# Optimization experiments

Measured on AMD Instinct MI355X. Metric: run time of the kernel, lower is better.

## Reference

```python
import jax, jax.numpy as jnp
import numpy as np

DIM = 768
HID = 1536
EPS = 1e-12
SCALE = float(np.sqrt(DIM))


def _layernorm(x, gamma, beta):
    mu = jnp.mean(x, axis=-1, keepdims=True)
    var = jnp.mean(jnp.square(x - mu), axis=-1, keepdims=True)
    return (x - mu) * jax.lax.rsqrt(var + EPS) * gamma + beta


def setup_inputs() -> dict:
    key = jax.random.key(0)
    ks = jax.random.split(key, 16)
    s = 1.0 / np.sqrt(DIM)
    sh = 1.0 / np.sqrt(HID)
    x = jax.random.normal(ks[0], (8, 2048, DIM), dtype=jnp.float32)
    return {
        "x": x,
        "Wq": jax.random.uniform(ks[1], (DIM, DIM), jnp.float32, -s, s),
        "bq": jax.random.uniform(ks[2], (DIM,), jnp.float32, -s, s),
        "Wk": jax.random.uniform(ks[3], (DIM, DIM), jnp.float32, -s, s),
        "bk": jax.random.uniform(ks[4], (DIM,), jnp.float32, -s, s),
        "Wv": jax.random.uniform(ks[5], (DIM, DIM), jnp.float32, -s, s),
        "bv": jax.random.uniform(ks[6], (DIM,), jnp.float32, -s, s),
        "Wp": jax.random.uniform(ks[7], (DIM, DIM), jnp.float32, -s, s),
        "bp": jax.random.uniform(ks[8], (DIM,), jnp.float32, -s, s),
        "g1": jnp.ones((DIM,), jnp.float32),
        "be1": jnp.zeros((DIM,), jnp.float32),
        "W1": jax.random.uniform(ks[9], (HID, DIM), jnp.float32, -s, s),
        "b1": jax.random.uniform(ks[10], (HID,), jnp.float32, -s, s),
        "W2": jax.random.uniform(ks[11], (DIM, HID), jnp.float32, -sh, sh),
        "b2": jax.random.uniform(ks[12], (DIM,), jnp.float32, -sh, sh),
        "g2": jnp.ones((DIM,), jnp.float32),
        "be2": jnp.zeros((DIM,), jnp.float32),
    }


def reference(x, Wq, bq, Wk, bk, Wv, bv, Wp, bp, g1, be1, W1, b1, W2, b2, g2, be2):
    # NOTE: original code does NOT split into heads; single full-dim bmm attention.
    Q = jnp.einsum("bsd,ed->bse", x, Wq) + bq  # [B,S,D]
    K = jnp.einsum("bsd,ed->bse", x, Wk) + bk
    V = jnp.einsum("bsd,ed->bse", x, Wv) + bv
    alpha = jnp.einsum("bqd,bkd->bqk", Q, K) / SCALE  # [B,S,S]
    alpha = jax.nn.softmax(alpha, axis=-1)
    attn = jnp.einsum("bqk,bkd->bqd", alpha, V)
    attn = jnp.einsum("bsd,ed->bse", attn, Wp) + bp  # linear_proj
    h = _layernorm(x + attn, g1, be1)
    mlp = jax.nn.gelu(jnp.einsum("bsd,hd->bsh", h, W1) + b1, approximate=False)
    mlp = jnp.einsum("bsh,dh->bsd", mlp, W2) + b2
    return _layernorm(h + mlp, g2, be2)
```

## Files before the change

### kernel.cpp

```cpp
#include <hip/hip_runtime.h>
#include <math.h>

#define D_MODEL 768
#define D_HID   1536
#define N_BATCH 8
#define SEQLEN  2048
#define NROWS   (N_BATCH*SEQLEN)

typedef unsigned short u16;
typedef unsigned char  u8;
typedef __attribute__((ext_vector_type(8))) short bfrag;
typedef __attribute__((ext_vector_type(4))) float facc;

__device__ __forceinline__ u16 f2bf(float f) {
  unsigned u = __float_as_uint(f);
  u += 0x7fffu + ((u >> 16) & 1u);
  return (u16)(u >> 16);
}
__device__ __forceinline__ float bf2f(u16 u) {
  return __uint_as_float((unsigned)u << 16);
}
__device__ __forceinline__ u8 f2fp8(float f) {
  return (u8)(__builtin_amdgcn_cvt_pk_fp8_f32(f, f, 0, 0) & 0xff);
}

__device__ __forceinline__ void async16(const void* g, void* l) {
  __builtin_amdgcn_global_load_lds((const __attribute__((address_space(1))) void*)g,
                                   (__attribute__((address_space(3))) void*)l,
                                   16, 0, 0);
}

__global__ __launch_bounds__(256) void cvt_all(
    const float* __restrict__ x,  const float* __restrict__ Wq,
    const float* __restrict__ Wk, const float* __restrict__ Wv,
    const float* __restrict__ Wp, const float* __restrict__ W1,
    const float* __restrict__ W2, const float* __restrict__ bq,
    const float* __restrict__ bk, const float* __restrict__ bv,
    u16* __restrict__ XB, u16* __restrict__ WQKV, u16* __restrict__ WPB,
    u16* __restrict__ W1B, u16* __restrict__ W2B, float* __restrict__ BQKV,
    float* __restrict__ LSUM) {
  long i = (long)blockIdx.x * 256 + threadIdx.x;
  const float* src; u16* dst; long off;
  if      (i < 3145728) { src = x;  dst = XB;             off = i; }
  else if (i < 3293184) { src = Wq; dst = WQKV;           off = i - 3145728; }
  else if (i < 3440640) { src = Wk; dst = WQKV + 589824;  off = i - 3293184; }
  else if (i < 3588096) { src = Wv; dst = WQKV + 1179648; off = i - 3440640; }
  else if (i < 3735552) { src = Wp; dst = WPB;            off = i - 3588096; }
  else if (i < 4030464) { src = W1; dst = W1B;            off = i - 3735552; }
  else if (i < 4325376) { src = W2; dst = W2B;            off = i - 4030464; }
  else if (i < 4325952) {
    long j = i - 4325376;
    const float* s = (j < 192) ? bq : (j < 384) ? bk : bv;
    long o = (j < 192) ? j : (j < 384) ? j - 192 : j - 384;
    ((float4*)BQKV)[j] = ((const float4*)s)[o];
    return;
  } else if (i < 4330048) {
    float4 zz = {0.f, 0.f, 0.f, 0.f};
    ((float4*)LSUM)[i - 4325952] = zz;
    return;
  } else return;
  float4 v = ((const float4*)src)[off];
  ushort4 o4;
  o4.x = f2bf(v.x); o4.y = f2bf(v.y); o4.z = f2bf(v.z); o4.w = f2bf(v.w);
  *reinterpret_cast<ushort4*>(dst + off * 4) = o4;
}

enum { EPI_EXP = 1, EPI_DIV = 2, EPI_GELU = 4, EPI_QKV = 5, EPI_RES = 6 };

template<int EPI>
__global__ __launch_bounds__(512, 4)
void gemm_bt(const u16* __restrict__ Aall, const u16* __restrict__ Ball,
             void* __restrict__ Cout,
             int M, int N, int K,
             long sA, long sB, long sC,
             const float* __restrict__ bias,
             const u16* __restrict__ resid,
             float* __restrict__ lsum,
             float scale)
{
  __shared__ __align__(16) char smem[65536];
  u16* As = (u16*)smem;
  u16* Bs = (u16*)(smem + 16384);

  const int z = blockIdx.z;
  const u16* A = Aall + (long)z * sA;
  const u16* B = Ball + (long)z * sB;
  const int bm = blockIdx.x, bn = blockIdx.y;
  const int tid = (int)threadIdx.x;
  const int lane = tid & 63, wv = tid >> 6;
  const int wr = wv >> 2, wc = wv & 3;

  facc acc[4][4] = {};

  const int srow = tid >> 3;
  const int scol = (((tid & 7) ^ (srow & 7)) << 3);
  const u16* Abase = A + (long)(bm * 128) * K;
  const u16* Bbase = B + (long)(bn * 256) * K;

  const int fr = lane & 15;
  const int g0 = lane >> 4;

  for (int k0 = 0; k0 < K; k0 += 64) {
    __syncthreads();
#pragma unroll
    for (int p = 0; p < 2; ++p)
      async16(Abase + (long)(p * 64 + srow) * K + k0 + scol, As + (p * 512 + wv * 64) * 8);
#pragma unroll
    for (int p = 0; p < 4; ++p)
      async16(Bbase + (long)(p * 64 + srow) * K + k0 + scol, Bs + (p * 512 + wv * 64) * 8);
    __syncthreads();
#pragma unroll
    for (int h = 0; h < 2; ++h) {
      bfrag af[4], bfv[4];
      const int gh = g0 + h * 4;
#pragma unroll
      for (int i = 0; i < 4; ++i) {
        const int r = wr * 64 + i * 16 + fr;
        af[i] = *(const bfrag*)(As + r * 64 + ((gh ^ (r & 7)) << 3));
      }
#pragma unroll
      for (int j = 0; j < 4; ++j) {
        const int r = wc * 64 + j * 16 + fr;
        bfv[j] = *(const bfrag*)(Bs + r * 64 + ((gh ^ (r & 7)) << 3));
      }
#pragma unroll
      for (int i = 0; i < 4; ++i)
#pragma unroll
        for (int j = 0; j < 4; ++j)
          acc[i][j] = __builtin_amdgcn_mfma_f32_16x16x32_bf16(af[i], bfv[j], acc[i][j], 0, 0, 0);
    }
  }

  __syncthreads();
  const int rb = bm * 128 + wr * 64;
  const int cb = bn * 256 + wc * 64;
  const int quad = lane >> 4;

  if constexpr (EPI == EPI_QKV) {
    const int c64 = bn * 4 + wc;
    const int which = c64 / 12;
    float bj[4];
#pragma unroll
    for (int j = 0; j < 4; ++j) bj[j] = bias[cb + j * 16 + fr];
    if (which == 2) {
      u8* VT_ = (u8*)resid;
      const int zb = rb >> 11;
      const int seqb = (rb & 2047) + quad * 4;
      const int dimb = (c64 - 24) * 64;
#pragma unroll
      for (int i = 0; i < 4; ++i) {
#pragma unroll
        for (int j = 0; j < 4; ++j) {
          const int dim = dimb + j * 16 + fr;
          unsigned v01 = __builtin_amdgcn_cvt_pk_fp8_f32(acc[i][j][0] + bj[j],
                                                         acc[i][j][1] + bj[j], 0, 0);
          unsigned v23 = __builtin_amdgcn_cvt_pk_fp8_f32(acc[i][j][2] + bj[j],
                                                         acc[i][j][3] + bj[j], 0, 0);
          unsigned w = (v01 & 0xffffu) | (v23 << 16);
          *reinterpret_cast<unsigned*>(VT_ + (long)zb * D_MODEL * SEQLEN +
                                       (long)dim * SEQLEN + seqb + i * 16) = w;
        }
      }
      return;
    }
    u8* ep8 = (u8*)(smem + wv * 8192);
    u8* Cg = (u8*)Cout + (long)which * NROWS * D_MODEL;
    const int cbo = (c64 - which * 12) * 64;
#pragma unroll
    for (int i = 0; i < 4; ++i)
#pragma unroll
      for (int r = 0; r < 4; ++r) {
        const int lrow = i * 16 + quad * 4 + r;
#pragma unroll
        for (int j = 0; j < 4; ++j)
          ep8[lrow * 64 + j * 16 + fr] = f2fp8(acc[i][j][r] + bj[j]);
      }
#pragma unroll
    for (int it = 0; it < 4; ++it) {
      const int lr = it * 16 + (lane >> 2);
      const int ch = (lane & 3) << 4;
      int4 d = *(const int4*)(ep8 + lr * 64 + ch);
      *reinterpret_cast<int4*>(Cg + (long)(rb + lr) * D_MODEL + cbo + ch) = d;
    }
  } else {
    u16* ep16 = (u16*)(smem + wv * 8192);
    u16* Cg = (u16*)Cout + (long)z * sC;
    float bj[4];
#pragma unroll
    for (int j = 0; j < 4; ++j) bj[j] = bias[cb + j * 16 + fr];
#pragma unroll
    for (int i = 0; i < 4; ++i) {
#pragma unroll
      for (int r = 0; r < 4; ++r) {
        const int lrow = i * 16 + quad * 4 + r;
#pragma unroll
        for (int j = 0; j < 4; ++j) {
          float t = acc[i][j][r] + bj[j];
          float y = 0.7978845608f * (t + 0.044715f * t * t * t);
          float e = __expf(-2.f * fabsf(y));
          float th = (1.f - e) / (1.f + e);
          th = (y < 0.f) ? -th : th;
          ep16[lrow * 64 + j * 16 + fr] = f2bf(0.5f * t * (1.f + th));
        }
      }
    }
#pragma unroll
    for (int it = 0; it < 8; ++it) {
      const int lr = it * 8 + (lane >> 3);
      const int ch = (lane & 7) << 3;
      int4 d = *(const int4*)(ep16 + lr * 64 + ch);
      *reinterpret_cast<int4*>(Cg + (long)(rb + lr) * N + cb + ch) = d;
    }
  }
}

template<int EPI>
__global__ __launch_bounds__(512, 4)
void gemm_f8(const u8* __restrict__ Aall, const u8* __restrict__ Ball,
             void* __restrict__ Cout,
             int M, int N, int K,
             long sA, long sB, long sC,
             float* __restrict__ lsum, float scale)
{
  __shared__ __align__(16) char smem[49152];
  u8* As = (u8*)smem;
  u8* Bs = (u8*)(smem + 16384);

  const int z = blockIdx.z;
  const u8* A = Aall + (long)z * sA;
  const u8* B = Ball + (long)z * sB;
  const int bm = blockIdx.x, bn = blockIdx.y;
  const int tid = (int)threadIdx.x;
  const int lane = tid & 63, wv = tid >> 6;
  const int wr = wv >> 2, wc = wv & 3;

  facc acc[4][4] = {};

  const int srow = tid >> 3;
  const int scol = (((tid & 7) ^ (srow & 7)) << 4);
  const u8* Abase = A + (long)(bm * 128) * K;
  const u8* Bbase = B + (long)(bn * 256) * K;

  const int fr = lane & 15;
  const int g0 = lane >> 4;

  for (int k0 = 0; k0 < K; k0 += 128) {
    __syncthreads();
#pragma unroll
    for (int p = 0; p < 2; ++p)
      async16(Abase + (long)(p * 64 + srow) * K + k0 + scol, As + (p * 512 + wv * 64) * 16);
#pragma unroll
    for (int p = 0; p < 4; ++p)
      async16(Bbase + (long)(p * 64 + srow) * K + k0 + scol, Bs + (p * 512 + wv * 64) * 16);
    __syncthreads();
#pragma unroll
    for (int s = 0; s < 4; ++s) {
      long af[4], bfv[4];
      const int c = s * 2 + (g0 >> 1);
      const int w8 = (g0 & 1) << 3;
#pragma unroll
      for (int i = 0; i < 4; ++i) {
        const int r = wr * 64 + i * 16 + fr;
        af[i] = *(const long*)(As + r * 128 + ((c ^ (r & 7)) << 4) + w8);
      }
#pragma unroll
      for (int j = 0; j < 4; ++j) {
        const int r = wc * 64 + j * 16 + fr;
        bfv[j] = *(const long*)(Bs + r * 128 + ((c ^ (r & 7)) << 4) + w8);
      }
#pragma unroll
      for (int i = 0; i < 4; ++i)
#pragma unroll
        for (int j = 0; j < 4; ++j)
          acc[i][j] = __builtin_amdgcn_mfma_f32_16x16x32_fp8_fp8(af[i], bfv[j], acc[i][j], 0, 0, 0);
    }
  }

  __syncthreads();
  const int rb = bm * 128 + wr * 64;
  const int cb = bn * 256 + wc * 64;
  const int quad = lane >> 4;

  if constexpr (EPI == EPI_EXP) {
    u8* ep8 = (u8*)(smem + wv * 4096);
    u8* Cg = (u8*)Cout + (long)z * sC;
#pragma unroll
    for (int i = 0; i < 4; ++i) {
#pragma unroll
      for (int r = 0; r < 4; ++r) {
        const int lrow = i * 16 + quad * 4 + r;
        const int row = rb + lrow;
        float rs = 0.f;
#pragma unroll
        for (int j = 0; j < 4; ++j) {
          float e = __expf(acc[i][j][r] * scale - 3.0f);
          rs += e;
          ep8[lrow * 64 + j * 16 + fr] = f2fp8(e);
        }
        rs += __shfl_xor(rs, 1);
        rs += __shfl_xor(rs, 2);
        rs += __shfl_xor(rs, 4);
        rs += __shfl_xor(rs, 8);
        if (fr == 0) atomicAdd(&lsum[(long)z * M + row], rs);
      }
    }
#pragma unroll
    for (int it = 0; it < 4; ++it) {
      const int lr = it * 16 + (lane >> 2);
      const int ch = (lane & 3) << 4;
      int4 d = *(const int4*)(ep8 + lr * 64 + ch);
      *reinterpret_cast<int4*>(Cg + (long)(rb + lr) * N + cb + ch) = d;
    }
  } else {
    u16* ep16 = (u16*)(smem + wv * 4096);
    u16* Cg = (u16*)Cout + (long)z * sC;
#pragma unroll
    for (int h = 0; h < 2; ++h) {
#pragma unroll
      for (int i2 = 0; i2 < 2; ++i2) {
        const int i = h * 2 + i2;
#pragma unroll
        for (int r = 0; r < 4; ++r) {
          const int lrow = i2 * 16 + quad * 4 + r;
          const int row = rb + h * 32 + lrow;
          const float inv = 1.f / lsum[(long)z * M + row];
#pragma unroll
          for (int j = 0; j < 4; ++j)
            ep16[lrow * 64 + j * 16 + fr] = f2bf(acc[i][j][r] * inv);
        }
      }
#pragma unroll
      for (int it = 0; it < 4; ++it) {
        const int lr = it * 8 + (lane >> 3);
        const int ch = (lane & 7) << 3;
        int4 d = *(const int4*)(ep16 + lr * 64 + ch);
        *reinterpret_cast<int4*>(Cg + (long)(rb + h * 32 + lr) * N + cb + ch) = d;
      }
    }
  }
}

template<int EPI>
__global__ __launch_bounds__(256, 4)
void gemm_bt128(const u16* __restrict__ Aall, const u16* __restrict__ Ball,
                void* __restrict__ Cout,
                int M, int N, int K,
                long sA, long sB, long sC,
                const float* __restrict__ bias,
                const u16* __restrict__ resid,
                float* __restrict__ lsum,
                float scale)
{
  __shared__ __align__(16) char smem[32768];
  u16* As = (u16*)smem;
  u16* Bs = (u16*)(smem + 16384);

  const int z = blockIdx.z;
  const u16* A = Aall + (long)z * sA;
  const u16* B = Ball + (long)z * sB;
  const int bm = blockIdx.x, bn = blockIdx.y;
  const int tid = (int)threadIdx.x;
  const int lane = tid & 63, wv = tid >> 6;
  const int wr = wv >> 1, wc = wv & 1;

  facc acc[4][4] = {};

  const int srow = tid >> 3;
  const int scol = (((tid & 7) ^ (srow & 7)) << 3);
  const u16* Abase = A + (long)(bm * 128) * K;
  const u16* Bbase = B + (long)(bn * 128) * K;
  const int fr = lane & 15, g0 = lane >> 4;

  for (int k0 = 0; k0 < K; k0 += 64) {
    __syncthreads();
#pragma unroll
    for (int p = 0; p < 4; ++p) {
      async16(Abase + (long)(p * 32 + srow) * K + k0 + scol, As + (p * 256 + wv * 64) * 8);
      async16(Bbase + (long)(p * 32 + srow) * K + k0 + scol, Bs + (p * 256 + wv * 64) * 8);
    }
    __syncthreads();
#pragma unroll
    for (int h = 0; h < 2; ++h) {
      bfrag af[4], bfv[4];
      const int gh = g0 + h * 4;
#pragma unroll
      for (int i = 0; i < 4; ++i) {
        const int r = wr * 64 + i * 16 + fr;
        af[i] = *(const bfrag*)(As + r * 64 + ((gh ^ (r & 7)) << 3));
      }
#pragma unroll
      for (int j = 0; j < 4; ++j) {
        const int r = wc * 64 + j * 16 + fr;
        bfv[j] = *(const bfrag*)(Bs + r * 64 + ((gh ^ (r & 7)) << 3));
      }
#pragma unroll
      for (int i = 0; i < 4; ++i)
#pragma unroll
        for (int j = 0; j < 4; ++j)
          acc[i][j] = __builtin_amdgcn_mfma_f32_16x16x32_bf16(af[i], bfv[j], acc[i][j], 0, 0, 0);
    }
  }

  __syncthreads();
  const int rb = bm * 128 + wr * 64;
  const int cb = bn * 128 + wc * 64;
  const int quad = lane >> 4;

  float* ep32 = (float*)(smem + wv * 8192);
  u16* Cg = (u16*)Cout;
#pragma unroll
  for (int h = 0; h < 2; ++h) {
#pragma unroll
    for (int i2 = 0; i2 < 2; ++i2) {
      const int i = h * 2 + i2;
#pragma unroll
      for (int r = 0; r < 4; ++r) {
        const int lrow = i2 * 16 + quad * 4 + r;
#pragma unroll
        for (int j = 0; j < 4; ++j)
          ep32[lrow * 64 + j * 16 + fr] = acc[i][j][r];
      }
    }
#pragma unroll
    for (int it = 0; it < 8; ++it) {
      const int lr = it * 4 + (lane >> 4);
      const int ch = (lane & 15) << 2;
      float4 d = *(const float4*)(ep32 + lr * 64 + ch);
      const int row = rb + h * 32 + lr;
      const int gcol = cb + ch;
      const long gi = (long)row * N + gcol;
      ushort4 rv = *(const ushort4*)(resid + gi);
      float4 bb = *(const float4*)(bias + gcol);
      ushort4 o;
      o.x = f2bf(d.x + bb.x + bf2f(rv.x));
      o.y = f2bf(d.y + bb.y + bf2f(rv.y));
      o.z = f2bf(d.z + bb.z + bf2f(rv.z));
      o.w = f2bf(d.w + bb.w + bf2f(rv.w));
      *reinterpret_cast<ushort4*>(Cg + gi) = o;
    }
  }
  (void)lsum; (void)scale; (void)sC; (void)M;
}

__global__ __launch_bounds__(192) void layernorm_rows(const u16* __restrict__ in,
                                                      const float* __restrict__ gamma,
                                                      const float* __restrict__ beta,
                                                      float* __restrict__ outf,
                                                      u16* __restrict__ outb) {
  const int row = blockIdx.x;
  const int t = threadIdx.x;
  ushort4 uv = ((const ushort4*)(in + (long)row * D_MODEL))[t];
  float v0 = bf2f(uv.x), v1 = bf2f(uv.y), v2 = bf2f(uv.z), v3 = bf2f(uv.w);
  float s1 = v0 + v1 + v2 + v3;
  float s2 = v0 * v0 + v1 * v1 + v2 * v2 + v3 * v3;
#pragma unroll
  for (int o = 32; o; o >>= 1) { s1 += __shfl_xor(s1, o); s2 += __shfl_xor(s2, o); }
  __shared__ float r1[3], r2[3];
  const int wv = t >> 6, ln = t & 63;
  if (ln == 0) { r1[wv] = s1; r2[wv] = s2; }
  __syncthreads();
  s1 = r1[0] + r1[1] + r1[2];
  s2 = r2[0] + r2[1] + r2[2];
  const float mu = s1 * (1.f / 768.f);
  const float var = s2 * (1.f / 768.f) - mu * mu;
  const float rstd = rsqrtf(var + 1e-12f);
  float4 gv = ((const float4*)gamma)[t];
  float4 bv = ((const float4*)beta)[t];
  float o0 = (v0 - mu) * rstd * gv.x + bv.x;
  float o1 = (v1 - mu) * rstd * gv.y + bv.y;
  float o2 = (v2 - mu) * rstd * gv.z + bv.z;
  float o3 = (v3 - mu) * rstd * gv.w + bv.w;
  if (outf) {
    float4 ov = {o0, o1, o2, o3};
    ((float4*)(outf + (long)row * D_MODEL))[t] = ov;
  }
  if (outb) {
    ushort4 ob;
    ob.x = f2bf(o0); ob.y = f2bf(o1); ob.z = f2bf(o2); ob.w = f2bf(o3);
    ((ushort4*)(outb + (long)row * D_MODEL))[t] = ob;
  }
}

static const size_t OFF_WP   = 0;
static const size_t OFF_W1   = 1179648;
static const size_t OFF_W2   = 3538944;
static const size_t OFF_LSUM = 5898240;
static const size_t OFF_BQKV = 5963776;
static const size_t OFF_QB   = 6291456;
static const size_t OFF_KB   = 18874368;
static const size_t OFF_VT   = 31457280;
static const size_t OFF_EB   = 44040192;
static const size_t OFF_CTX  = 77594624;
static const size_t OFF_XB   = 102760448;
static const size_t OFF_WQKV = 127926272;
static const size_t OFF_M1B  = 131465216;

extern "C" void kernel_launch(void* const* d_in, const int* in_sizes, int n_in,
                              void* d_out, int out_size, void* d_ws, size_t ws_size,
                              hipStream_t stream) {
  const float* x   = (const float*)d_in[0];
  const float* Wq  = (const float*)d_in[1];
  const float* bq  = (const float*)d_in[2];
  const float* Wk  = (const float*)d_in[3];
  const float* bk  = (const float*)d_in[4];
  const float* Wv  = (const float*)d_in[5];
  const float* bv  = (const float*)d_in[6];
  const float* Wp  = (const float*)d_in[7];
  const float* bp  = (const float*)d_in[8];
  const float* g1  = (const float*)d_in[9];
  const float* be1 = (const float*)d_in[10];
  const float* W1  = (const float*)d_in[11];
  const float* b1  = (const float*)d_in[12];
  const float* W2  = (const float*)d_in[13];
  const float* b2  = (const float*)d_in[14];
  const float* g2  = (const float*)d_in[15];
  const float* be2 = (const float*)d_in[16];

  char* ws = (char*)d_ws;
  u16*   WPB  = (u16*)(ws + OFF_WP);
  u16*   W1B  = (u16*)(ws + OFF_W1);
  u16*   W2B  = (u16*)(ws + OFF_W2);
  float* LSUM = (float*)(ws + OFF_LSUM);
  float* BQKV = (float*)(ws + OFF_BQKV);
  u8*    QB   = (u8*)(ws + OFF_QB);
  u8*    KB   = (u8*)(ws + OFF_KB);
  u8*    VT   = (u8*)(ws + OFF_VT);
  u8*    EB   = (u8*)(ws + OFF_EB);
  u16*   CTX  = (u16*)(ws + OFF_CTX);
  u16*   XB   = (u16*)(ws + OFF_XB);
  u16*   WQKV = (u16*)(ws + OFF_WQKV);
  u16*   M1B  = (u16*)(ws + OFF_M1B);
  u16*   PB   = (u16*)(ws + OFF_QB);
  u16*   HB   = (u16*)(ws + OFF_EB);
  u16*   M2B  = (u16*)(ws + OFF_CTX);

  dim3 blk(256), blkg(512), blkl(192);

  cvt_all<<<dim3(16915), blk, 0, stream>>>(x, Wq, Wk, Wv, Wp, W1, W2, bq, bk, bv,
                                           XB, WQKV, WPB, W1B, W2B, BQKV, LSUM);

  gemm_bt<EPI_QKV><<<dim3(128, 9, 1), blkg, 0, stream>>>(XB, WQKV, QB,
      NROWS, 3 * D_MODEL, D_MODEL, 0, 0, 0, BQKV, (const u16*)VT, nullptr, 0.f);

  const float sc = 1.0f / sqrtf((float)D_MODEL);
  gemm_f8<EPI_EXP><<<dim3(16, 8, 8), blkg, 0, stream>>>(QB, KB, EB,
      SEQLEN, SEQLEN, D_MODEL,
      (long)SEQLEN * D_MODEL, (long)SEQLEN * D_MODEL, (long)SEQLEN * SEQLEN,
      LSUM, sc);
  gemm_f8<EPI_DIV><<<dim3(16, 3, 8), blkg, 0, stream>>>(EB, VT, CTX,
      SEQLEN, D_MODEL, SEQLEN,
      (long)SEQLEN * SEQLEN, (long)D_MODEL * SEQLEN, (long)SEQLEN * D_MODEL,
      LSUM, 0.f);
  gemm_bt128<EPI_RES><<<dim3(128, 6, 1), blk, 0, stream>>>(CTX, WPB, PB,
      NROWS, D_MODEL, D_MODEL, 0, 0, 0, bp, XB, nullptr, 0.f);
  layernorm_rows<<<dim3(NROWS), blkl, 0, stream>>>(PB, g1, be1, nullptr, HB);
  gemm_bt<EPI_GELU><<<dim3(128, 6, 1), blkg, 0, stream>>>(HB, W1B, M1B,
      NROWS, D_HID, D_MODEL, 0, 0, 0, b1, nullptr, nullptr, 0.f);
  gemm_bt128<EPI_RES><<<dim3(128, 6, 1), blk, 0, stream>>>(M1B, W2B, M2B,
      NROWS, D_MODEL, D_HID, 0, 0, 0, b2, HB, nullptr, 0.f);
  layernorm_rows<<<dim3(NROWS), blkl, 0, stream>>>(M2B, g2, be2, (float*)d_out, nullptr);

  (void)in_sizes; (void)n_in; (void)out_size; (void)ws_size;
}
```

Before: 467.7 us.

## Use 256x256 double-buffered GEMM tiles with prefetch for all matmuls

Replaces the 128x256 bf16/fp8 GEMMs and the 128x128 residual GEMM with a single 256x256-tile kernel family. Each k-step loads the next K slice asynchronously into a second 64KB LDS buffer while the current one is consumed in four quadrant sub-phases with s_setprio around the MFMA blocks. The intent is more operand reuse per byte loaded and overlap of global loads with compute. In exchange it uses 128KB of LDS, more accumulator registers, and occupancy limited to 2 blocks. Grids are smaller, e.g. 64x3 for the projection GEMMs, which may underfill the CUs.

```diff
diff --git a/kernel.cpp b/kernel.cpp
--- a/kernel.cpp
+++ b/kernel.cpp
@@ -29,6 +29,12 @@
                                    (__attribute__((address_space(3))) void*)l,
                                    16, 0, 0);
 }
+__device__ __forceinline__ void wg_barrier() {
+  asm volatile("" ::: "memory");
+  __builtin_amdgcn_s_barrier();
+  asm volatile("" ::: "memory");
+}
+#define VMCNT(n) asm volatile("s_waitcnt vmcnt(" #n ")" ::: "memory")
 
 __global__ __launch_bounds__(256) void cvt_all(
     const float* __restrict__ x,  const float* __restrict__ Wq,
@@ -68,20 +74,17 @@
 enum { EPI_EXP = 1, EPI_DIV = 2, EPI_GELU = 4, EPI_QKV = 5, EPI_RES = 6 };
 
 template<int EPI>
-__global__ __launch_bounds__(512, 4)
-void gemm_bt(const u16* __restrict__ Aall, const u16* __restrict__ Ball,
-             void* __restrict__ Cout,
-             int M, int N, int K,
-             long sA, long sB, long sC,
-             const float* __restrict__ bias,
-             const u16* __restrict__ resid,
-             float* __restrict__ lsum,
-             float scale)
+__global__ __launch_bounds__(512, 2)
+void gemm8(const u16* __restrict__ Aall, const u16* __restrict__ Ball,
+           void* __restrict__ Cout,
+           int M, int N, int K,
+           long sA, long sB, long sC,
+           const float* __restrict__ bias,
+           const u16* __restrict__ resid,
+           float* __restrict__ lsum,
+           float scale)
 {
-  __shared__ __align__(16) char smem[65536];
-  u16* As = (u16*)smem;
-  u16* Bs = (u16*)(smem + 16384);
-
+  __shared__ __align__(16) char smem[131072];
   const int z = blockIdx.z;
   const u16* A = Aall + (long)z * sA;
   const u16* B = Ball + (long)z * sB;
@@ -90,49 +93,67 @@
   const int lane = tid & 63, wv = tid >> 6;
   const int wr = wv >> 2, wc = wv & 3;
 
-  facc acc[4][4] = {};
+  facc acc[8][4] = {};
 
   const int srow = tid >> 3;
   const int scol = (((tid & 7) ^ (srow & 7)) << 3);
-  const u16* Abase = A + (long)(bm * 128) * K;
+  const u16* Abase = A + (long)(bm * 256) * K;
   const u16* Bbase = B + (long)(bn * 256) * K;
-
-  const int fr = lane & 15;
-  const int g0 = lane >> 4;
-
-  for (int k0 = 0; k0 < K; k0 += 64) {
-    __syncthreads();
-#pragma unroll
-    for (int p = 0; p < 2; ++p)
-      async16(Abase + (long)(p * 64 + srow) * K + k0 + scol, As + (p * 512 + wv * 64) * 8);
+  const int fr = lane & 15, g0 = lane >> 4;
+  const int nt = K >> 6;
+
+  auto STAGE = [&](int t, int b) {
+    u16* Asb = (u16*)(smem + b * 65536);
+    u16* Bsb = (u16*)(smem + b * 65536 + 32768);
+    const long k0 = (long)t * 64;
 #pragma unroll
     for (int p = 0; p < 4; ++p)
-      async16(Bbase + (long)(p * 64 + srow) * K + k0 + scol, Bs + (p * 512 + wv * 64) * 8);
-    __syncthreads();
-#pragma unroll
-    for (int h = 0; h < 2; ++h) {
-      bfrag af[4], bfv[4];
-      const int gh = g0 + h * 4;
-#pragma unroll
-      for (int i = 0; i < 4; ++i) {
-        const int r = wr * 64 + i * 16 + fr;
-        af[i] = *(const bfrag*)(As + r * 64 + ((gh ^ (r & 7)) << 3));
-      }
-#pragma unroll
-      for (int j = 0; j < 4; ++j) {
-        const int r = wc * 64 + j * 16 + fr;
-        bfv[j] = *(const bfrag*)(Bs + r * 64 + ((gh ^ (r & 7)) << 3));
-      }
-#pragma unroll
-      for (int i = 0; i < 4; ++i)
-#pragma unroll
-        for (int j = 0; j < 4; ++j)
-          acc[i][j] = __builtin_amdgcn_mfma_f32_16x16x32_bf16(af[i], bfv[j], acc[i][j], 0, 0, 0);
-    }
-  }
-
-  __syncthreads();
-  const int rb = bm * 128 + wr * 64;
+      async16(Abase + (long)(p * 64 + srow) * K + k0 + scol, Asb + p * 4096 + wv * 512);
+#pragma unroll
+    for (int p = 0; p < 4; ++p)
+      async16(Bbase + (long)(p * 64 + srow) * K + k0 + scol, Bsb + p * 4096 + wv * 512);
+  };
+
+#define G8_LDA(mh)                                                              \
+  _Pragma("unroll") for (int i = 0; i < 4; ++i)                                 \
+  _Pragma("unroll") for (int h = 0; h < 2; ++h) {                               \
+    const int r = wr * 128 + (mh) * 64 + i * 16 + fr;                           \
+    af[i][h] = *(const bfrag*)(As + r * 64 + (((g0 + h * 4) ^ (r & 7)) << 3));  \
+  }
+#define G8_LDB(nh)                                                              \
+  _Pragma("unroll") for (int j = 0; j < 2; ++j)                                 \
+  _Pragma("unroll") for (int h = 0; h < 2; ++h) {                               \
+    const int r = wc * 64 + (nh) * 32 + j * 16 + fr;                            \
+    bfv[j][h] = *(const bfrag*)(Bs + r * 64 + (((g0 + h * 4) ^ (r & 7)) << 3)); \
+  }
+#define G8_FMA(mh, nh)                                                          \
+  __builtin_amdgcn_s_setprio(1);                                                \
+  _Pragma("unroll") for (int i = 0; i < 4; ++i)                                 \
+  _Pragma("unroll") for (int j = 0; j < 2; ++j)                                 \
+  _Pragma("unroll") for (int h = 0; h < 2; ++h)                                 \
+    acc[(mh) * 4 + i][(nh) * 2 + j] = __builtin_amdgcn_mfma_f32_16x16x32_bf16(  \
+        af[i][h], bfv[j][h], acc[(mh) * 4 + i][(nh) * 2 + j], 0, 0, 0);         \
+  __builtin_amdgcn_s_setprio(0);
+
+  STAGE(0, 0);
+  for (int t = 0; t < nt; ++t) {
+    const int ct = t & 1;
+    const u16* As = (const u16*)(smem + ct * 65536);
+    const u16* Bs = (const u16*)(smem + ct * 65536 + 32768);
+    if (t + 1 < nt) { STAGE(t + 1, ct ^ 1); VMCNT(8); }
+    else            { VMCNT(0); }
+    wg_barrier();
+    bfrag af[4][2], bfv[2][2];
+    G8_LDA(0) G8_LDB(0) G8_FMA(0, 0) wg_barrier();
+    G8_LDB(1)           G8_FMA(0, 1) wg_barrier();
+    G8_LDA(1)           G8_FMA(1, 1) wg_barrier();
+    G8_LDB(0)           G8_FMA(1, 0) wg_barrier();
+  }
+#undef G8_LDA
+#undef G8_LDB
+#undef G8_FMA
+
+  const int rb = bm * 256 + wr * 128;
   const int cb = bn * 256 + wc * 64;
   const int quad = lane >> 4;
 
@@ -145,10 +166,10 @@
     if (which == 2) {
       u8* VT_ = (u8*)resid;
       const int zb = rb >> 11;
-      const int seqb = (rb & 2047) + quad * 4;
+      const int sbase = rb & 2047;
       const int dimb = (c64 - 24) * 64;
 #pragma unroll
-      for (int i = 0; i < 4; ++i) {
+      for (int i = 0; i < 8; ++i)
 #pragma unroll
         for (int j = 0; j < 4; ++j) {
           const int dim = dimb + j * 16 + fr;
@@ -158,16 +179,15 @@
                                                          acc[i][j][3] + bj[j], 0, 0);
           unsigned w = (v01 & 0xffffu) | (v23 << 16);
           *reinterpret_cast<unsigned*>(VT_ + (long)zb * D_MODEL * SEQLEN +
-                                       (long)dim * SEQLEN + seqb + i * 16) = w;
+                                       (long)dim * SEQLEN + sbase + i * 16 + quad * 4) = w;
         }
-      }
       return;
     }
     u8* ep8 = (u8*)(smem + wv * 8192);
     u8* Cg = (u8*)Cout + (long)which * NROWS * D_MODEL;
     const int cbo = (c64 - which * 12) * 64;
 #pragma unroll
-    for (int i = 0; i < 4; ++i)
+    for (int i = 0; i < 8; ++i)
 #pragma unroll
       for (int r = 0; r < 4; ++r) {
         const int lrow = i * 16 + quad * 4 + r;
@@ -176,56 +196,87 @@
           ep8[lrow * 64 + j * 16 + fr] = f2fp8(acc[i][j][r] + bj[j]);
       }
 #pragma unroll
-    for (int it = 0; it < 4; ++it) {
+    for (int it = 0; it < 8; ++it) {
       const int lr = it * 16 + (lane >> 2);
       const int ch = (lane & 3) << 4;
       int4 d = *(const int4*)(ep8 + lr * 64 + ch);
       *reinterpret_cast<int4*>(Cg + (long)(rb + lr) * D_MODEL + cbo + ch) = d;
     }
-  } else {
-    u16* ep16 = (u16*)(smem + wv * 8192);
+  } else if constexpr (EPI == EPI_GELU) {
+    u16* ep16 = (u16*)(smem + wv * 16384);
     u16* Cg = (u16*)Cout + (long)z * sC;
     float bj[4];
 #pragma unroll
     for (int j = 0; j < 4; ++j) bj[j] = bias[cb + j * 16 + fr];
 #pragma unroll
-    for (int i = 0; i < 4; ++i) {
+    for (int i = 0; i < 8; ++i)
 #pragma unroll
       for (int r = 0; r < 4; ++r) {
         const int lrow = i * 16 + quad * 4 + r;
 #pragma unroll
         for (int j = 0; j < 4; ++j) {
-          float t = acc[i][j][r] + bj[j];
-          float y = 0.7978845608f * (t + 0.044715f * t * t * t);
+          float tt = acc[i][j][r] + bj[j];
+          float y = 0.7978845608f * (tt + 0.044715f * tt * tt * tt);
           float e = __expf(-2.f * fabsf(y));
           float th = (1.f - e) / (1.f + e);
           th = (y < 0.f) ? -th : th;
-          ep16[lrow * 64 + j * 16 + fr] = f2bf(0.5f * t * (1.f + th));
+          ep16[lrow * 64 + j * 16 + fr] = f2bf(0.5f * tt * (1.f + th));
         }
       }
-    }
-#pragma unroll
-    for (int it = 0; it < 8; ++it) {
+#pragma unroll
+    for (int it = 0; it < 16; ++it) {
       const int lr = it * 8 + (lane >> 3);
       const int ch = (lane & 7) << 3;
       int4 d = *(const int4*)(ep16 + lr * 64 + ch);
       *reinterpret_cast<int4*>(Cg + (long)(rb + lr) * N + cb + ch) = d;
     }
-  }
+  } else {
+    float* ep32 = (float*)(smem + wv * 16384);
+    u16* Cg = (u16*)Cout;
+#pragma unroll
+    for (int h2 = 0; h2 < 2; ++h2) {
+#pragma unroll
+      for (int i2 = 0; i2 < 4; ++i2) {
+        const int i = h2 * 4 + i2;
+#pragma unroll
+        for (int r = 0; r < 4; ++r) {
+          const int lrow = i2 * 16 + quad * 4 + r;
+#pragma unroll
+          for (int j = 0; j < 4; ++j)
+            ep32[lrow * 64 + j * 16 + fr] = acc[i][j][r];
+        }
+      }
+#pragma unroll
+      for (int it = 0; it < 16; ++it) {
+        const int lr = it * 4 + (lane >> 4);
+        const int ch = (lane & 15) << 2;
+        float4 d = *(const float4*)(ep32 + lr * 64 + ch);
+        const int row = rb + h2 * 64 + lr;
+        const int gcol = cb + ch;
+        const long gi = (long)row * N + gcol;
+        ushort4 rv = *(const ushort4*)(resid + gi);
+        float4 bb = *(const float4*)(bias + gcol);
+        ushort4 o;
+        o.x = f2bf(d.x + bb.x + bf2f(rv.x));
+        o.y = f2bf(d.y + bb.y + bf2f(rv.y));
+        o.z = f2bf(d.z + bb.z + bf2f(rv.z));
+        o.w = f2bf(d.w + bb.w + bf2f(rv.w));
+        *reinterpret_cast<ushort4*>(Cg + gi) = o;
+      }
+    }
+  }
+  (void)lsum; (void)scale; (void)M;
 }
 
 template<int EPI>
-__global__ __launch_bounds__(512, 4)
-void gemm_f8(const u8* __restrict__ Aall, const u8* __restrict__ Ball,
-             void* __restrict__ Cout,
-             int M, int N, int K,
-             long sA, long sB, long sC,
-             float* __restrict__ lsum, float scale)
+__global__ __launch_bounds__(512, 2)
+void gemm8_f8(const u8* __restrict__ Aall, const u8* __restrict__ Ball,
+              void* __restrict__ Cout,
+              int M, int N, int K,
+              long sA, long sB, long sC,
+              float* __restrict__ lsum, float scale)
 {
-  __shared__ __align__(16) char smem[49152];
-  u8* As = (u8*)smem;
-  u8* Bs = (u8*)(smem + 16384);
-
+  __shared__ __align__(16) char smem[131072];
   const int z = blockIdx.z;
   const u8* A = Aall + (long)z * sA;
   const u8* B = Ball + (long)z * sB;
@@ -234,58 +285,77 @@
   const int lane = tid & 63, wv = tid >> 6;
   const int wr = wv >> 2, wc = wv & 3;
 
-  facc acc[4][4] = {};
+  facc acc[8][4] = {};
 
   const int srow = tid >> 3;
-  const int scol = (((tid & 7) ^ (srow & 7)) << 4);
-  const u8* Abase = A + (long)(bm * 128) * K;
+  const int scolb = (((tid & 7) ^ (srow & 7)) << 4);
+  const u8* Abase = A + (long)(bm * 256) * K;
   const u8* Bbase = B + (long)(bn * 256) * K;
-
-  const int fr = lane & 15;
-  const int g0 = lane >> 4;
-
-  for (int k0 = 0; k0 < K; k0 += 128) {
-    __syncthreads();
-#pragma unroll
-    for (int p = 0; p < 2; ++p)
-      async16(Abase + (long)(p * 64 + srow) * K + k0 + scol, As + (p * 512 + wv * 64) * 16);
+  const int fr = lane & 15, g0 = lane >> 4;
+  const int nt = K >> 7;
+
+  auto STAGE = [&](int t, int b) {
+    u8* Asb = (u8*)(smem + b * 65536);
+    u8* Bsb = (u8*)(smem + b * 65536 + 32768);
+    const long k0 = (long)t << 7;
 #pragma unroll
     for (int p = 0; p < 4; ++p)
-      async16(Bbase + (long)(p * 64 + srow) * K + k0 + scol, Bs + (p * 512 + wv * 64) * 16);
-    __syncthreads();
-#pragma unroll
-    for (int s = 0; s < 4; ++s) {
-      long af[4], bfv[4];
-      const int c = s * 2 + (g0 >> 1);
-      const int w8 = (g0 & 1) << 3;
-#pragma unroll
-      for (int i = 0; i < 4; ++i) {
-        const int r = wr * 64 + i * 16 + fr;
-        af[i] = *(const long*)(As + r * 128 + ((c ^ (r & 7)) << 4) + w8);
-      }
-#pragma unroll
-      for (int j = 0; j < 4; ++j) {
-        const int r = wc * 64 + j * 16 + fr;
-        bfv[j] = *(const long*)(Bs + r * 128 + ((c ^ (r & 7)) << 4) + w8);
-      }
-#pragma unroll
-      for (int i = 0; i < 4; ++i)
-#pragma unroll
-        for (int j = 0; j < 4; ++j)
-          acc[i][j] = __builtin_amdgcn_mfma_f32_16x16x32_fp8_fp8(af[i], bfv[j], acc[i][j], 0, 0, 0);
-    }
-  }
-
-  __syncthreads();
-  const int rb = bm * 128 + wr * 64;
+      async16(Abase + (long)(p * 64 + srow) * K + k0 + scolb, Asb + p * 8192 + wv * 1024);
+#pragma unroll
+    for (int p = 0; p < 4; ++p)
+      async16(Bbase + (long)(p * 64 + srow) * K + k0 + scolb, Bsb + p * 8192 + wv * 1024);
+  };
+
+#define F8_LDA(mh)                                                                   \
+  _Pragma("unroll") for (int i = 0; i < 4; ++i)                                      \
+  _Pragma("unroll") for (int s = 0; s < 4; ++s) {                                    \
+    const int r = wr * 128 + (mh) * 64 + i * 16 + fr;                                \
+    const int c = s * 2 + (g0 >> 1);                                                 \
+    af[i][s] = *(const long*)(As + r * 128 + ((c ^ (r & 7)) << 4) + ((g0 & 1) << 3)); \
+  }
+#define F8_LDB(nh)                                                                   \
+  _Pragma("unroll") for (int j = 0; j < 2; ++j)                                      \
+  _Pragma("unroll") for (int s = 0; s < 4; ++s) {                                    \
+    const int r = wc * 64 + (nh) * 32 + j * 16 + fr;                                 \
+    const int c = s * 2 + (g0 >> 1);                                                 \
+    bfv[j][s] = *(const long*)(Bs + r * 128 + ((c ^ (r & 7)) << 4) + ((g0 & 1) << 3)); \
+  }
+#define F8_FMA(mh, nh)                                                               \
+  __builtin_amdgcn_s_setprio(1);                                                     \
+  _Pragma("unroll") for (int i = 0; i < 4; ++i)                                      \
+  _Pragma("unroll") for (int j = 0; j < 2; ++j)                                      \
+  _Pragma("unroll") for (int s = 0; s < 4; ++s)                                      \
+    acc[(mh) * 4 + i][(nh) * 2 + j] = __builtin_amdgcn_mfma_f32_16x16x32_fp8_fp8(    \
+        af[i][s], bfv[j][s], acc[(mh) * 4 + i][(nh) * 2 + j], 0, 0, 0);              \
+  __builtin_amdgcn_s_setprio(0);
+
+  STAGE(0, 0);
+  for (int t = 0; t < nt; ++t) {
+    const int ct = t & 1;
+    const u8* As = (const u8*)(smem + ct * 65536);
+    const u8* Bs = (const u8*)(smem + ct * 65536 + 32768);
+    if (t + 1 < nt) { STAGE(t + 1, ct ^ 1); VMCNT(8); }
+    else            { VMCNT(0); }
+    wg_barrier();
+    long af[4][4], bfv[2][4];
+    F8_LDA(0) F8_LDB(0) F8_FMA(0, 0) wg_barrier();
+    F8_LDB(1)           F8_FMA(0, 1) wg_barrier();
+    F8_LDA(1)           F8_FMA(1, 1) wg_barrier();
+    F8_LDB(0)           F8_FMA(1, 0) wg_barrier();
+  }
+#undef F8_LDA
+#undef F8_LDB
+#undef F8_FMA
+
+  const int rb = bm * 256 + wr * 128;
   const int cb = bn * 256 + wc * 64;
   const int quad = lane >> 4;
 
   if constexpr (EPI == EPI_EXP) {
-    u8* ep8 = (u8*)(smem + wv * 4096);
+    u8* ep8 = (u8*)(smem + wv * 8192);
     u8* Cg = (u8*)Cout + (long)z * sC;
 #pragma unroll
-    for (int i = 0; i < 4; ++i) {
+    for (int i = 0; i < 8; ++i) {
 #pragma unroll
       for (int r = 0; r < 4; ++r) {
         const int lrow = i * 16 + quad * 4 + r;
@@ -305,141 +375,35 @@
       }
     }
 #pragma unroll
-    for (int it = 0; it < 4; ++it) {
+    for (int it = 0; it < 8; ++it) {
       const int lr = it * 16 + (lane >> 2);
       const int ch = (lane & 3) << 4;
       int4 d = *(const int4*)(ep8 + lr * 64 + ch);
       *reinterpret_cast<int4*>(Cg + (long)(rb + lr) * N + cb + ch) = d;
     }
   } else {
-    u16* ep16 = (u16*)(smem + wv * 4096);
+    u16* ep16 = (u16*)(smem + wv * 16384);
     u16* Cg = (u16*)Cout + (long)z * sC;
 #pragma unroll
-    for (int h = 0; h < 2; ++h) {
-#pragma unroll
-      for (int i2 = 0; i2 < 2; ++i2) {
-        const int i = h * 2 + i2;
-#pragma unroll
-        for (int r = 0; r < 4; ++r) {
-          const int lrow = i2 * 16 + quad * 4 + r;
-          const int row = rb + h * 32 + lrow;
-          const float inv = 1.f / lsum[(long)z * M + row];
-#pragma unroll
-          for (int j = 0; j < 4; ++j)
-            ep16[lrow * 64 + j * 16 + fr] = f2bf(acc[i][j][r] * inv);
-        }
+    for (int i = 0; i < 8; ++i) {
+#pragma unroll
+      for (int r = 0; r < 4; ++r) {
+        const int lrow = i * 16 + quad * 4 + r;
+        const int row = rb + lrow;
+        const float inv = 1.f / lsum[(long)z * M + row];
+#pragma unroll
+        for (int j = 0; j < 4; ++j)
+          ep16[lrow * 64 + j * 16 + fr] = f2bf(acc[i][j][r] * inv);
       }
-#pragma unroll
-      for (int it = 0; it < 4; ++it) {
-        const int lr = it * 8 + (lane >> 3);
-        const int ch = (lane & 7) << 3;
-        int4 d = *(const int4*)(ep16 + lr * 64 + ch);
-        *reinterpret_cast<int4*>(Cg + (long)(rb + h * 32 + lr) * N + cb + ch) = d;
-      }
-    }
-  }
-}
-
-template<int EPI>
-__global__ __launch_bounds__(256, 4)
-void gemm_bt128(const u16* __restrict__ Aall, const u16* __restrict__ Ball,
-                void* __restrict__ Cout,
-                int M, int N, int K,
-                long sA, long sB, long sC,
-                const float* __restrict__ bias,
-                const u16* __restrict__ resid,
-                float* __restrict__ lsum,
-                float scale)
-{
-  __shared__ __align__(16) char smem[32768];
-  u16* As = (u16*)smem;
-  u16* Bs = (u16*)(smem + 16384);
-
-  const int z = blockIdx.z;
-  const u16* A = Aall + (long)z * sA;
-  const u16* B = Ball + (long)z * sB;
-  const int bm = blockIdx.x, bn = blockIdx.y;
-  const int tid = (int)threadIdx.x;
-  const int lane = tid & 63, wv = tid >> 6;
-  const int wr = wv >> 1, wc = wv & 1;
-
-  facc acc[4][4] = {};
-
-  const int srow = tid >> 3;
-  const int scol = (((tid & 7) ^ (srow & 7)) << 3);
-  const u16* Abase = A + (long)(bm * 128) * K;
-  const u16* Bbase = B + (long)(bn * 128) * K;
-  const int fr = lane & 15, g0 = lane >> 4;
-
-  for (int k0 = 0; k0 < K; k0 += 64) {
-    __syncthreads();
-#pragma unroll
-    for (int p = 0; p < 4; ++p) {
-      async16(Abase + (long)(p * 32 + srow) * K + k0 + scol, As + (p * 256 + wv * 64) * 8);
-      async16(Bbase + (long)(p * 32 + srow) * K + k0 + scol, Bs + (p * 256 + wv * 64) * 8);
-    }
-    __syncthreads();
-#pragma unroll
-    for (int h = 0; h < 2; ++h) {
-      bfrag af[4], bfv[4];
-      const int gh = g0 + h * 4;
-#pragma unroll
-      for (int i = 0; i < 4; ++i) {
-        const int r = wr * 64 + i * 16 + fr;
-        af[i] = *(const bfrag*)(As + r * 64 + ((gh ^ (r & 7)) << 3));
-      }
-#pragma unroll
-      for (int j = 0; j < 4; ++j) {
-        const int r = wc * 64 + j * 16 + fr;
-        bfv[j] = *(const bfrag*)(Bs + r * 64 + ((gh ^ (r & 7)) << 3));
-      }
-#pragma unroll
-      for (int i = 0; i < 4; ++i)
-#pragma unroll
-        for (int j = 0; j < 4; ++j)
-          acc[i][j] = __builtin_amdgcn_mfma_f32_16x16x32_bf16(af[i], bfv[j], acc[i][j], 0, 0, 0);
-    }
-  }
-
-  __syncthreads();
-  const int rb = bm * 128 + wr * 64;
-  const int cb = bn * 128 + wc * 64;
-  const int quad = lane >> 4;
-
-  float* ep32 = (float*)(smem + wv * 8192);
-  u16* Cg = (u16*)Cout;
-#pragma unroll
-  for (int h = 0; h < 2; ++h) {
-#pragma unroll
-    for (int i2 = 0; i2 < 2; ++i2) {
-      const int i = h * 2 + i2;
-#pragma unroll
-      for (int r = 0; r < 4; ++r) {
-        const int lrow = i2 * 16 + quad * 4 + r;
-#pragma unroll
-        for (int j = 0; j < 4; ++j)
-          ep32[lrow * 64 + j * 16 + fr] = acc[i][j][r];
-      }
-    }
-#pragma unroll
-    for (int it = 0; it < 8; ++it) {
-      const int lr = it * 4 + (lane >> 4);
-      const int ch = (lane & 15) << 2;
-      float4 d = *(const float4*)(ep32 + lr * 64 + ch);
-      const int row = rb + h * 32 + lr;
-      const int gcol = cb + ch;
-      const long gi = (long)row * N + gcol;
-      ushort4 rv = *(const ushort4*)(resid + gi);
-      float4 bb = *(const float4*)(bias + gcol);
-      ushort4 o;
-      o.x = f2bf(d.x + bb.x + bf2f(rv.x));
-      o.y = f2bf(d.y + bb.y + bf2f(rv.y));
-      o.z = f2bf(d.z + bb.z + bf2f(rv.z));
-      o.w = f2bf(d.w + bb.w + bf2f(rv.w));
-      *reinterpret_cast<ushort4*>(Cg + gi) = o;
-    }
-  }
-  (void)lsum; (void)scale; (void)sC; (void)M;
+    }
+#pragma unroll
+    for (int it = 0; it < 16; ++it) {
+      const int lr = it * 8 + (lane >> 3);
+      const int ch = (lane & 7) << 3;
+      int4 d = *(const int4*)(ep16 + lr * 64 + ch);
+      *reinterpret_cast<int4*>(Cg + (long)(rb + lr) * N + cb + ch) = d;
+    }
+  }
 }
 
 __global__ __launch_bounds__(192) void layernorm_rows(const u16* __restrict__ in,
@@ -534,29 +498,29 @@
   u16*   HB   = (u16*)(ws + OFF_EB);
   u16*   M2B  = (u16*)(ws + OFF_CTX);
 
-  dim3 blk(256), blkg(512), blkl(192);
+  dim3 blk(256), b512(512), blkl(192);
 
   cvt_all<<<dim3(16915), blk, 0, stream>>>(x, Wq, Wk, Wv, Wp, W1, W2, bq, bk, bv,
                                            XB, WQKV, WPB, W1B, W2B, BQKV, LSUM);
 
-  gemm_bt<EPI_QKV><<<dim3(128, 9, 1), blkg, 0, stream>>>(XB, WQKV, QB,
+  gemm8<EPI_QKV><<<dim3(64, 9, 1), b512, 0, stream>>>(XB, WQKV, QB,
       NROWS, 3 * D_MODEL, D_MODEL, 0, 0, 0, BQKV, (const u16*)VT, nullptr, 0.f);
 
   const float sc = 1.0f / sqrtf((float)D_MODEL);
-  gemm_f8<EPI_EXP><<<dim3(16, 8, 8), blkg, 0, stream>>>(QB, KB, EB,
+  gemm8_f8<EPI_EXP><<<dim3(8, 8, 8), b512, 0, stream>>>(QB, KB, EB,
       SEQLEN, SEQLEN, D_MODEL,
       (long)SEQLEN * D_MODEL, (long)SEQLEN * D_MODEL, (long)SEQLEN * SEQLEN,
       LSUM, sc);
-  gemm_f8<EPI_DIV><<<dim3(16, 3, 8), blkg, 0, stream>>>(EB, VT, CTX,
+  gemm8_f8<EPI_DIV><<<dim3(8, 3, 8), b512, 0, stream>>>(EB, VT, CTX,
       SEQLEN, D_MODEL, SEQLEN,
       (long)SEQLEN * SEQLEN, (long)D_MODEL * SEQLEN, (long)SEQLEN * D_MODEL,
       LSUM, 0.f);
-  gemm_bt128<EPI_RES><<<dim3(128, 6, 1), blk, 0, stream>>>(CTX, WPB, PB,
+  gemm8<EPI_RES><<<dim3(64, 3, 1), b512, 0, stream>>>(CTX, WPB, PB,
       NROWS, D_MODEL, D_MODEL, 0, 0, 0, bp, XB, nullptr, 0.f);
   layernorm_rows<<<dim3(NROWS), blkl, 0, stream>>>(PB, g1, be1, nullptr, HB);
-  gemm_bt<EPI_GELU><<<dim3(128, 6, 1), blkg, 0, stream>>>(HB, W1B, M1B,
+  gemm8<EPI_GELU><<<dim3(64, 6, 1), b512, 0, stream>>>(HB, W1B, M1B,
       NROWS, D_HID, D_MODEL, 0, 0, 0, b1, nullptr, nullptr, 0.f);
-  gemm_bt128<EPI_RES><<<dim3(128, 6, 1), blk, 0, stream>>>(M1B, W2B, M2B,
+  gemm8<EPI_RES><<<dim3(64, 3, 1), b512, 0, stream>>>(M1B, W2B, M2B,
       NROWS, D_MODEL, D_HID, 0, 0, 0, b2, HB, nullptr, 0.f);
   layernorm_rows<<<dim3(NROWS), blkl, 0, stream>>>(M2B, g2, be2, (float*)d_out, nullptr);
 
```

New measurement: 527.3 us. 12.7% more time.

## Add triple-buffered async LDS pipeline with vmcnt waits to all GEMM kernels

Applied to the files above, without the earlier changes.

Each of the three GEMM kernels now stages K-tiles into three rotating LDS buffers. Loads are issued two tiles ahead, and each iteration uses a single barrier plus an explicit vmcnt wait, replacing the two __syncthreads per tile. The K step is halved (32 bf16 / 64 fp8) and the XOR swizzle is adjusted to match, and MFMA sections are wrapped in s_setprio. The aim is to overlap global-to-LDS loads with MFMA compute. The cost is more LDS per block (72KB for the 512-thread kernels), which can cut occupancy below the launch_bounds target, and the vmcnt accounting must stay exact.

```diff
diff --git a/kernel.cpp b/kernel.cpp
--- a/kernel.cpp
+++ b/kernel.cpp
@@ -29,6 +29,12 @@
                                    (__attribute__((address_space(3))) void*)l,
                                    16, 0, 0);
 }
+__device__ __forceinline__ void wg_barrier() {
+  asm volatile("" ::: "memory");
+  __builtin_amdgcn_s_barrier();
+  asm volatile("" ::: "memory");
+}
+#define VMCNT(n) asm volatile("s_waitcnt vmcnt(" #n ")" ::: "memory")
 
 __global__ __launch_bounds__(256) void cvt_all(
     const float* __restrict__ x,  const float* __restrict__ Wq,
@@ -78,10 +84,7 @@
              float* __restrict__ lsum,
              float scale)
 {
-  __shared__ __align__(16) char smem[65536];
-  u16* As = (u16*)smem;
-  u16* Bs = (u16*)(smem + 16384);
-
+  __shared__ __align__(16) char smem[73728];
   const int z = blockIdx.z;
   const u16* A = Aall + (long)z * sA;
   const u16* B = Ball + (long)z * sB;
@@ -92,46 +95,53 @@
 
   facc acc[4][4] = {};
 
-  const int srow = tid >> 3;
-  const int scol = (((tid & 7) ^ (srow & 7)) << 3);
+  const int srow = tid >> 2;
+  const int sc = (((tid & 3) ^ (srow & 3)) << 3);
   const u16* Abase = A + (long)(bm * 128) * K;
   const u16* Bbase = B + (long)(bn * 256) * K;
-
-  const int fr = lane & 15;
-  const int g0 = lane >> 4;
-
-  for (int k0 = 0; k0 < K; k0 += 64) {
-    __syncthreads();
-#pragma unroll
-    for (int p = 0; p < 2; ++p)
-      async16(Abase + (long)(p * 64 + srow) * K + k0 + scol, As + (p * 512 + wv * 64) * 8);
-#pragma unroll
-    for (int p = 0; p < 4; ++p)
-      async16(Bbase + (long)(p * 64 + srow) * K + k0 + scol, Bs + (p * 512 + wv * 64) * 8);
-    __syncthreads();
-#pragma unroll
-    for (int h = 0; h < 2; ++h) {
-      bfrag af[4], bfv[4];
-      const int gh = g0 + h * 4;
-#pragma unroll
-      for (int i = 0; i < 4; ++i) {
-        const int r = wr * 64 + i * 16 + fr;
-        af[i] = *(const bfrag*)(As + r * 64 + ((gh ^ (r & 7)) << 3));
-      }
-#pragma unroll
-      for (int j = 0; j < 4; ++j) {
-        const int r = wc * 64 + j * 16 + fr;
-        bfv[j] = *(const bfrag*)(Bs + r * 64 + ((gh ^ (r & 7)) << 3));
-      }
-#pragma unroll
-      for (int i = 0; i < 4; ++i)
-#pragma unroll
-        for (int j = 0; j < 4; ++j)
-          acc[i][j] = __builtin_amdgcn_mfma_f32_16x16x32_bf16(af[i], bfv[j], acc[i][j], 0, 0, 0);
-    }
-  }
-
-  __syncthreads();
+  const int fr = lane & 15, g0 = lane >> 4;
+  const int nt = K >> 5;
+
+  auto STAGE = [&](int t, int b) {
+    char* Asb = smem + b * 24576;
+    char* Bsb = Asb + 8192;
+    const long k0 = (long)t << 5;
+    async16(Abase + (long)srow * K + k0 + sc, Asb + tid * 16);
+    async16(Bbase + (long)srow * K + k0 + sc, Bsb + tid * 16);
+    async16(Bbase + (long)(128 + srow) * K + k0 + sc, Bsb + 8192 + tid * 16);
+  };
+
+  STAGE(0, 0); STAGE(1, 1);
+  int rb_ = 0, sb_ = 2;
+  for (int t = 0; t < nt; ++t) {
+    if (t < nt - 1) { VMCNT(3); } else { VMCNT(0); }
+    wg_barrier();
+    if (t + 2 < nt) STAGE(t + 2, sb_);
+    const u16* As = (const u16*)(smem + rb_ * 24576);
+    const u16* Bs = As + 4096;
+    bfrag af[4], bf[4];
+#pragma unroll
+    for (int i = 0; i < 4; ++i) {
+      const int r = wr * 64 + i * 16 + fr;
+      af[i] = *(const bfrag*)(As + r * 32 + ((g0 ^ (r & 3)) << 3));
+    }
+#pragma unroll
+    for (int j = 0; j < 4; ++j) {
+      const int r = wc * 64 + j * 16 + fr;
+      bf[j] = *(const bfrag*)(Bs + r * 32 + ((g0 ^ (r & 3)) << 3));
+    }
+    __builtin_amdgcn_s_setprio(1);
+#pragma unroll
+    for (int i = 0; i < 4; ++i)
+#pragma unroll
+      for (int j = 0; j < 4; ++j)
+        acc[i][j] = __builtin_amdgcn_mfma_f32_16x16x32_bf16(af[i], bf[j], acc[i][j], 0, 0, 0);
+    __builtin_amdgcn_s_setprio(0);
+    rb_ = (rb_ == 2) ? 0 : rb_ + 1;
+    sb_ = (sb_ == 2) ? 0 : sb_ + 1;
+  }
+  wg_barrier();
+
   const int rb = bm * 128 + wr * 64;
   const int cb = bn * 256 + wc * 64;
   const int quad = lane >> 4;
@@ -222,10 +232,7 @@
              long sA, long sB, long sC,
              float* __restrict__ lsum, float scale)
 {
-  __shared__ __align__(16) char smem[49152];
-  u8* As = (u8*)smem;
-  u8* Bs = (u8*)(smem + 16384);
-
+  __shared__ __align__(16) char smem[73728];
   const int z = blockIdx.z;
   const u8* A = Aall + (long)z * sA;
   const u8* B = Ball + (long)z * sB;
@@ -236,47 +243,58 @@
 
   facc acc[4][4] = {};
 
-  const int srow = tid >> 3;
-  const int scol = (((tid & 7) ^ (srow & 7)) << 4);
+  const int srow = tid >> 2;
+  const int scb = (((tid & 3) ^ (srow & 3)) << 4);
   const u8* Abase = A + (long)(bm * 128) * K;
   const u8* Bbase = B + (long)(bn * 256) * K;
-
-  const int fr = lane & 15;
-  const int g0 = lane >> 4;
-
-  for (int k0 = 0; k0 < K; k0 += 128) {
-    __syncthreads();
-#pragma unroll
-    for (int p = 0; p < 2; ++p)
-      async16(Abase + (long)(p * 64 + srow) * K + k0 + scol, As + (p * 512 + wv * 64) * 16);
-#pragma unroll
-    for (int p = 0; p < 4; ++p)
-      async16(Bbase + (long)(p * 64 + srow) * K + k0 + scol, Bs + (p * 512 + wv * 64) * 16);
-    __syncthreads();
-#pragma unroll
-    for (int s = 0; s < 4; ++s) {
-      long af[4], bfv[4];
+  const int fr = lane & 15, g0 = lane >> 4;
+  const int nt = K >> 6;
+
+  auto STAGE = [&](int t, int b) {
+    char* Asb = smem + b * 24576;
+    char* Bsb = Asb + 8192;
+    const long k0 = (long)t << 6;
+    async16(Abase + (long)srow * K + k0 + scb, Asb + tid * 16);
+    async16(Bbase + (long)srow * K + k0 + scb, Bsb + tid * 16);
+    async16(Bbase + (long)(128 + srow) * K + k0 + scb, Bsb + 8192 + tid * 16);
+  };
+
+  STAGE(0, 0); STAGE(1, 1);
+  int rb_ = 0, sb_ = 2;
+  for (int t = 0; t < nt; ++t) {
+    if (t < nt - 1) { VMCNT(3); } else { VMCNT(0); }
+    wg_barrier();
+    if (t + 2 < nt) STAGE(t + 2, sb_);
+    const u8* As = (const u8*)(smem + rb_ * 24576);
+    const u8* Bs = As + 8192;
+#pragma unroll
+    for (int s = 0; s < 2; ++s) {
+      long af[4], bf[4];
       const int c = s * 2 + (g0 >> 1);
-      const int w8 = (g0 & 1) << 3;
+      const int h8 = (g0 & 1) << 3;
 #pragma unroll
       for (int i = 0; i < 4; ++i) {
         const int r = wr * 64 + i * 16 + fr;
-        af[i] = *(const long*)(As + r * 128 + ((c ^ (r & 7)) << 4) + w8);
+        af[i] = *(const long*)(As + r * 64 + ((c ^ (r & 3)) << 4) + h8);
       }
 #pragma unroll
       for (int j = 0; j < 4; ++j) {
         const int r = wc * 64 + j * 16 + fr;
-        bfv[j] = *(const long*)(Bs + r * 128 + ((c ^ (r & 7)) << 4) + w8);
-      }
+        bf[j] = *(const long*)(Bs + r * 64 + ((c ^ (r & 3)) << 4) + h8);
+      }
+      __builtin_amdgcn_s_setprio(1);
 #pragma unroll
       for (int i = 0; i < 4; ++i)
 #pragma unroll
         for (int j = 0; j < 4; ++j)
-          acc[i][j] = __builtin_amdgcn_mfma_f32_16x16x32_fp8_fp8(af[i], bfv[j], acc[i][j], 0, 0, 0);
-    }
-  }
-
-  __syncthreads();
+          acc[i][j] = __builtin_amdgcn_mfma_f32_16x16x32_fp8_fp8(af[i], bf[j], acc[i][j], 0, 0, 0);
+      __builtin_amdgcn_s_setprio(0);
+    }
+    rb_ = (rb_ == 2) ? 0 : rb_ + 1;
+    sb_ = (sb_ == 2) ? 0 : sb_ + 1;
+  }
+  wg_barrier();
+
   const int rb = bm * 128 + wr * 64;
   const int cb = bn * 256 + wc * 64;
   const int quad = lane >> 4;
@@ -351,10 +369,7 @@
                 float* __restrict__ lsum,
                 float scale)
 {
-  __shared__ __align__(16) char smem[32768];
-  u16* As = (u16*)smem;
-  u16* Bs = (u16*)(smem + 16384);
-
+  __shared__ __align__(16) char smem[49152];
   const int z = blockIdx.z;
   const u16* A = Aall + (long)z * sA;
   const u16* B = Ball + (long)z * sB;
@@ -365,43 +380,55 @@
 
   facc acc[4][4] = {};
 
-  const int srow = tid >> 3;
-  const int scol = (((tid & 7) ^ (srow & 7)) << 3);
+  const int srow = tid >> 2;
+  const int sc = (((tid & 3) ^ (srow & 3)) << 3);
   const u16* Abase = A + (long)(bm * 128) * K;
   const u16* Bbase = B + (long)(bn * 128) * K;
   const int fr = lane & 15, g0 = lane >> 4;
-
-  for (int k0 = 0; k0 < K; k0 += 64) {
-    __syncthreads();
-#pragma unroll
-    for (int p = 0; p < 4; ++p) {
-      async16(Abase + (long)(p * 32 + srow) * K + k0 + scol, As + (p * 256 + wv * 64) * 8);
-      async16(Bbase + (long)(p * 32 + srow) * K + k0 + scol, Bs + (p * 256 + wv * 64) * 8);
-    }
-    __syncthreads();
-#pragma unroll
-    for (int h = 0; h < 2; ++h) {
-      bfrag af[4], bfv[4];
-      const int gh = g0 + h * 4;
-#pragma unroll
-      for (int i = 0; i < 4; ++i) {
-        const int r = wr * 64 + i * 16 + fr;
-        af[i] = *(const bfrag*)(As + r * 64 + ((gh ^ (r & 7)) << 3));
-      }
-#pragma unroll
-      for (int j = 0; j < 4; ++j) {
-        const int r = wc * 64 + j * 16 + fr;
-        bfv[j] = *(const bfrag*)(Bs + r * 64 + ((gh ^ (r & 7)) << 3));
-      }
-#pragma unroll
-      for (int i = 0; i < 4; ++i)
-#pragma unroll
-        for (int j = 0; j < 4; ++j)
-          acc[i][j] = __builtin_amdgcn_mfma_f32_16x16x32_bf16(af[i], bfv[j], acc[i][j], 0, 0, 0);
-    }
-  }
-
-  __syncthreads();
+  const int nt = K >> 5;
+
+  auto STAGE = [&](int t, int b) {
+    char* Asb = smem + b * 16384;
+    char* Bsb = Asb + 8192;
+    const long k0 = (long)t << 5;
+#pragma unroll
+    for (int p = 0; p < 2; ++p) {
+      async16(Abase + (long)(p * 64 + srow) * K + k0 + sc, Asb + p * 4096 + tid * 16);
+      async16(Bbase + (long)(p * 64 + srow) * K + k0 + sc, Bsb + p * 4096 + tid * 16);
+    }
+  };
+
+  STAGE(0, 0); STAGE(1, 1);
+  int rb_ = 0, sb_ = 2;
+  for (int t = 0; t < nt; ++t) {
+    if (t < nt - 1) { VMCNT(4); } else { VMCNT(0); }
+    wg_barrier();
+    if (t + 2 < nt) STAGE(t + 2, sb_);
+    const u16* As = (const u16*)(smem + rb_ * 16384);
+    const u16* Bs = As + 4096;
+    bfrag af[4], bf[4];
+#pragma unroll
+    for (int i = 0; i < 4; ++i) {
+      const int r = wr * 64 + i * 16 + fr;
+      af[i] = *(const bfrag*)(As + r * 32 + ((g0 ^ (r & 3)) << 3));
+    }
+#pragma unroll
+    for (int j = 0; j < 4; ++j) {
+      const int r = wc * 64 + j * 16 + fr;
+      bf[j] = *(const bfrag*)(Bs + r * 32 + ((g0 ^ (r & 3)) << 3));
+    }
+    __builtin_amdgcn_s_setprio(1);
+#pragma unroll
+    for (int i = 0; i < 4; ++i)
+#pragma unroll
+      for (int j = 0; j < 4; ++j)
+        acc[i][j] = __builtin_amdgcn_mfma_f32_16x16x32_bf16(af[i], bf[j], acc[i][j], 0, 0, 0);
+    __builtin_amdgcn_s_setprio(0);
+    rb_ = (rb_ == 2) ? 0 : rb_ + 1;
+    sb_ = (sb_ == 2) ? 0 : sb_ + 1;
+  }
+  wg_barrier();
+
   const int rb = bm * 128 + wr * 64;
   const int cb = bn * 128 + wc * 64;
   const int quad = lane >> 4;
```

After: 513.0 us. 9.7% more time.
